# Optimization experiments

Measured on AMD Instinct MI355X. Metric: run time of the kernel, lower is better.

Reference implementation:

```python
import jax, jax.numpy as jnp
import numpy as np

D = 64        # d_model
HEADS = 4
DH = D // HEADS   # 16 per-head dim (shared QK)
DEPTH = 4
NHASH = 4
BS = 64       # bucket_size
FF = 4 * D
SELF_ATTN_VAL = -5e4  # reformer-pytorch TOKEN_SELF_ATTN_VALUE


def layer_norm(x, g, b, eps=1e-5):
    m = x.mean(-1, keepdims=True)
    v = ((x - m) ** 2).mean(-1, keepdims=True)
    return (x - m) * jax.lax.rsqrt(v + eps) * g + b


def lsh_attention(x, wqk, wv, wo_w, wo_b, rot):
    # x: (B, L, D); rot: (DH, NHASH, n_buckets//2) fixed random rotations
    B, L, _ = x.shape
    nb = L // BS                       # n_buckets
    qk = x @ wqk                        # shared query/key projection, no bias
    v = x @ wv

    def split_heads(t):
        return t.reshape(B, L, HEADS, DH).transpose(0, 2, 1, 3).reshape(B * HEADS, L, DH)

    qk, v = split_heads(qk), split_heads(v)
    Bh = B * HEADS

    # --- LSH hashing: argmax over [rot, -rot] projections ---
    rotated = jnp.einsum('btf,fhi->bhti', qk, rot)          # (Bh, NHASH, L, nb//2)
    rotated = jnp.concatenate([rotated, -rotated], axis=-1)  # (Bh, NHASH, L, nb)
    buckets = jnp.argmax(rotated, axis=-1)                   # (Bh, NHASH, L)
    offsets = (jnp.arange(NHASH) * nb)[None, :, None]
    buckets = (buckets + offsets).reshape(Bh, NHASH * L)

    # --- sort tokens by (bucket, position) ---
    ticker = jnp.arange(NHASH * L)
    bkt_t = buckets * L + (ticker % L)[None, :]
    sticker = jnp.argsort(bkt_t, axis=-1)
    undo_sort = jnp.argsort(sticker, axis=-1)
    st = sticker % L                                          # (Bh, NHASH*L)

    sqk = jnp.take_along_axis(qk, st[..., None], axis=1)
    sv = jnp.take_along_axis(v, st[..., None], axis=1)

    n_chunks = NHASH * nb
    bq_t = st.reshape(Bh, n_chunks, BS)
    bqk = sqk.reshape(Bh, n_chunks, BS, DH)
    bv = sv.reshape(Bh, n_chunks, BS, DH)
    bq = bqk
    bk = bqk / jnp.maximum(jnp.linalg.norm(bqk, axis=-1, keepdims=True), 1e-12)

    def look_one_back(t):
        return jnp.concatenate([t, jnp.roll(t, 1, axis=1)], axis=2)

    bk = look_one_back(bk)                    # (Bh, n_chunks, 2*BS, DH)
    bv = look_one_back(bv)
    bkv_t = look_one_back(bq_t[..., None])[..., 0]  # (Bh, n_chunks, 2*BS)

    dots = jnp.einsum('bcie,bcje->bcij', bq, bk) * (DH ** -0.5)
    self_mask = bq_t[:, :, :, None] == bkv_t[:, :, None, :]
    dots = jnp.where(self_mask, SELF_ATTN_VAL, dots)

    lse = jax.scipy.special.logsumexp(dots, axis=-1, keepdims=True)
    probs = jnp.exp(dots - lse)
    bo = jnp.einsum('bcij,bcje->bcie', probs, bv)

    so = bo.reshape(Bh, NHASH * L, DH)
    slog = lse.reshape(Bh, NHASH * L)
    o = jnp.take_along_axis(so, undo_sort[..., None], axis=1).reshape(Bh, NHASH, L, DH)
    logits = jnp.take_along_axis(slog, undo_sort, axis=1).reshape(Bh, NHASH, L, 1)

    # combine hash rounds weighted by their softmax normalizers
    w = jnp.exp(logits - jax.scipy.special.logsumexp(logits, axis=1, keepdims=True))
    out = (o * w).sum(axis=1)                 # (Bh, L, DH)
    out = out.reshape(B, HEADS, L, DH).transpose(0, 2, 1, 3).reshape(B, L, D)
    return out @ wo_w + wo_b


def feed_forward(x, w1, b1, w2, b2):
    return jax.nn.gelu(x @ w1 + b1, approximate=False) @ w2 + b2


def setup_inputs() -> dict:
    key = jax.random.key(0)
    ks = jax.random.split(key, 12)
    B = 16
    s = 0.02
    nb = 1280 // BS  # 20 buckets at padded seq len
    return {
        'wave': jax.random.normal(ks[0], (B, 2, 1250), jnp.float32),
        'in_w': jax.random.normal(ks[1], (2, D), jnp.float32) * s,
        'in_b': jnp.zeros((D,), jnp.float32),
        'ln1_g': jnp.ones((DEPTH, D), jnp.float32),
        'ln1_b': jnp.zeros((DEPTH, D), jnp.float32),
        'wqk': jax.random.normal(ks[2], (DEPTH, D, D), jnp.float32) * s,
        'wv': jax.random.normal(ks[3], (DEPTH, D, D), jnp.float32) * s,
        'wo_w': jax.random.normal(ks[4], (DEPTH, D, D), jnp.float32) * s,
        'wo_b': jnp.zeros((DEPTH, D), jnp.float32),
        'rot': jax.random.normal(ks[5], (DEPTH, DH, NHASH, nb // 2), jnp.float32),
        'ln2_g': jnp.ones((DEPTH, D), jnp.float32),
        'ln2_b': jnp.zeros((DEPTH, D), jnp.float32),
        'w1': jax.random.normal(ks[6], (DEPTH, D, FF), jnp.float32) * s,
        'b1': jnp.zeros((DEPTH, FF), jnp.float32),
        'w2': jax.random.normal(ks[7], (DEPTH, FF, D), jnp.float32) * s,
        'b2': jnp.zeros((DEPTH, D), jnp.float32),
        'out_w': jax.random.normal(ks[8], (D, 1), jnp.float32) * s,
        'out_b': jnp.zeros((1,), jnp.float32),
    }


def reference(wave, in_w, in_b, ln1_g, ln1_b, wqk, wv, wo_w, wo_b, rot,
              ln2_g, ln2_b, w1, b1, w2, b2, out_w, out_b):
    x = wave.transpose(0, 2, 1)               # (B, 1250, 2)
    L0 = x.shape[1]
    pad = (-L0) % (BS * 2)                    # pad to multiple of 128 -> 1280
    x = jnp.pad(x, ((0, 0), (0, pad), (0, 0)))
    x = x @ in_w + in_b                       # (B, L, D)

    # reversible sequence: y1 = x1 + attn(LN(x2)); y2 = x2 + ff(LN(y1))
    x1 = x2 = x
    for i in range(DEPTH):
        x1 = x1 + lsh_attention(layer_norm(x2, ln1_g[i], ln1_b[i]),
                                wqk[i], wv[i], wo_w[i], wo_b[i], rot[i])
        x2 = x2 + feed_forward(layer_norm(x1, ln2_g[i], ln2_b[i]),
                               w1[i], b1[i], w2[i], b2[i])
    x = (x1 + x2) * 0.5
    y = (x @ out_w + out_b)[..., 0]
    return y[:, :L0]
```

## Files before the change

### kernel.cpp

```cpp
#include <hip/hip_runtime.h>
#include <math.h>

#define LSEQ 1280
#define L0SEQ 1250
#define DM 64
#define NHEADS 4
#define DHD 16
#define NHASH 4
#define NBUK 20
#define NCHUNK 80
#define FFD 256
#define NBATCH 16
#define NBH 64

#define XSZ (NBATCH*LSEQ*DM)
#define QKSZ (NBH*LSEQ*DHD)
#define OHSZ (NBH*NHASH*LSEQ*DHD)
#define SLSZ (NBH*NHASH*LSEQ)

typedef __attribute__((ext_vector_type(8))) short frag_ab;
typedef __attribute__((ext_vector_type(4))) float frag_c;

union FU4 { uint4 v; frag_ab f; };

__device__ __forceinline__ unsigned rnbf(float x){
    unsigned b = __float_as_uint(x);
    return (b + 0x7fffu + ((b >> 16) & 1u)) >> 16;
}
__device__ __forceinline__ float bf2f(unsigned h){ return __uint_as_float(h << 16); }
__device__ __forceinline__ unsigned rot16(unsigned x){ return (x >> 16) | (x << 16); }
__device__ __forceinline__ uint4 rot16v(uint4 a){
    uint4 r; r.x=rot16(a.x); r.y=rot16(a.y); r.z=rot16(a.z); r.w=rot16(a.w); return r;
}

__device__ __forceinline__ void split3(float x, unsigned& h, unsigned& m, unsigned& l){
    unsigned bx = __float_as_uint(x);
    h = bx >> 16;
    float r = x - __uint_as_float(bx & 0xffff0000u);
    unsigned br = __float_as_uint(r);
    m = br >> 16;
    float r2 = r - __uint_as_float(br & 0xffff0000u);
    l = __float_as_uint(r2) >> 16;
}

__global__ __launch_bounds__(256) void k_init(
    const float* __restrict__ wave, const float* __restrict__ in_w, const float* __restrict__ in_b,
    float* __restrict__ x1, float* __restrict__ x2,
    const float* __restrict__ wo_w, const float* __restrict__ w1,
    const float* __restrict__ w2, unsigned* __restrict__ wsplit)
{
    if (blockIdx.x < 5120) {
        int idx = blockIdx.x * 256 + threadIdx.x;
        int d = idx & 63;
        int t = idx >> 6;
        int b = t / LSEQ;
        int tt = t % LSEQ;
        float v0 = 0.f, v1 = 0.f;
        if (tt < L0SEQ) {
            v0 = wave[(size_t)(b*2+0)*L0SEQ + tt];
            v1 = wave[(size_t)(b*2+1)*L0SEQ + tt];
        }
        float x = v0 * in_w[d] + v1 * in_w[64 + d] + in_b[d];
        x1[idx] = x;
        x2[idx] = x;
    } else {
        int gid = (blockIdx.x - 5120) * 256 + threadIdx.x;
        int l = gid / 36864;
        int r = gid % 36864;
        float src; unsigned* dst; int idx; int stride;
        if (r < 4096) {
            int k = r >> 6, n = r & 63;
            src = wo_w[l*4096 + k*64 + n];
            dst = wsplit + l*8192;
            idx = (((k>>4)*4 + (n>>4))*16 + (n&15))*16 + (k&15);
            stride = 4096;
        } else if (r < 20480) {
            int rr = r - 4096;
            int k = rr >> 8, n = rr & 255;
            src = w1[l*16384 + k*256 + n];
            dst = wsplit + 32768 + l*32768;
            idx = (((k>>4)*16 + (n>>4))*16 + (n&15))*16 + (k&15);
            stride = 16384;
        } else {
            int rr = r - 20480;
            int k = rr >> 6, n = rr & 63;
            src = w2[l*16384 + k*64 + n];
            dst = wsplit + 163840 + l*32768;
            idx = (((k>>4)*4 + (n>>4))*16 + (n&15))*16 + (k&15);
            stride = 16384;
        }
        unsigned h, m, lo;
        split3(src, h, m, lo);
        dst[idx]          = h | (m<<16);
        dst[idx + stride] = lo | (h<<16);
    }
}

__global__ __launch_bounds__(256) void k_qkv(
    const float* __restrict__ x2, const float* __restrict__ g, const float* __restrict__ bta,
    const float* __restrict__ wqk, const float* __restrict__ wv, const float* __restrict__ rot,
    unsigned* __restrict__ qkvs, int* __restrict__ buckets)
{
    __shared__ float xln[16][68];
    __shared__ float qkt[16][68];
    __shared__ float vvt[16][68];
    __shared__ float rots[640];
    int tid = threadIdx.x;
    int b  = blockIdx.x / 80;
    int t0 = (blockIdx.x % 80) * 16;
    int tok = tid >> 4;
    int cg  = tid & 15;
    int c4  = cg * 4;

    for (int i = tid; i < 640; i += 256) rots[i] = rot[i];

    float4 xv4 = *(const float4*)&x2[((size_t)b*LSEQ + t0 + tok)*DM + c4];
    float s = xv4.x + xv4.y + xv4.z + xv4.w;
    float ss = xv4.x*xv4.x + xv4.y*xv4.y + xv4.z*xv4.z + xv4.w*xv4.w;
    s  += __shfl_xor(s,1);  s  += __shfl_xor(s,2);  s  += __shfl_xor(s,4);  s  += __shfl_xor(s,8);
    ss += __shfl_xor(ss,1); ss += __shfl_xor(ss,2); ss += __shfl_xor(ss,4); ss += __shfl_xor(ss,8);
    float m = s * (1.f/64.f);
    float vr = ss * (1.f/64.f) - m*m;
    float rstd = 1.f / sqrtf(vr + 1e-5f);
    {
        float4 g4 = *(const float4*)&g[c4];
        float4 b4 = *(const float4*)&bta[c4];
        float4 o;
        o.x = (xv4.x-m)*rstd*g4.x + b4.x;
        o.y = (xv4.y-m)*rstd*g4.y + b4.y;
        o.z = (xv4.z-m)*rstd*g4.z + b4.z;
        o.w = (xv4.w-m)*rstd*g4.w + b4.w;
        *(float4*)&xln[tok][c4] = o;
    }
    __syncthreads();

    float aq[4] = {0,0,0,0}, av[4] = {0,0,0,0};
    for (int f = 0; f < 64; f++) {
        float4 wq4 = *(const float4*)&wqk[f*64 + c4];
        float4 wv4 = *(const float4*)&wv [f*64 + c4];
        float xv = xln[tok][f];
        aq[0] += xv*wq4.x; aq[1] += xv*wq4.y; aq[2] += xv*wq4.z; aq[3] += xv*wq4.w;
        av[0] += xv*wv4.x; av[1] += xv*wv4.y; av[2] += xv*wv4.z; av[3] += xv*wv4.w;
    }
    *(float4*)&qkt[tok][c4] = *(float4*)aq;
    *(float4*)&vvt[tok][c4] = *(float4*)av;
    __syncthreads();

    int p = tid >> 2;
    int ptok = p >> 2, head = p & 3;
    int sub = tid & 3;
    int e0 = sub * 4;
    int t = t0 + ptok;
    float4 qf4 = *(const float4*)&qkt[ptok][head*16 + e0];
    float nsq = qf4.x*qf4.x + qf4.y*qf4.y + qf4.z*qf4.z + qf4.w*qf4.w;
    nsq += __shfl_xor(nsq,1); nsq += __shfl_xor(nsq,2);
    float inv = 1.f / fmaxf(sqrtf(nsq), 1e-12f);
    float qe[4] = {qf4.x, qf4.y, qf4.z, qf4.w};
    unsigned wq[4], wk[4];
    #pragma unroll
    for (int i=0;i<4;i++){
        float xq = qe[i]*0.25f;
        unsigned qh = rnbf(xq);
        unsigned ql = rnbf(xq - bf2f(qh));
        wq[i] = qh | (ql<<16);
        float xk = qe[i]*inv;
        unsigned kh = rnbf(xk);
        unsigned kl = rnbf(xk - bf2f(kh));
        wk[i] = kh | (kl<<16);
    }
    float4 vf4 = *(const float4*)&vvt[ptok][head*16 + e0];
    float ve[4] = {vf4.x, vf4.y, vf4.z, vf4.w};
    unsigned wv1[4], wv3[4];
    #pragma unroll
    for (int i=0;i<4;i++){
        unsigned vh_, vm_, vl_;
        split3(ve[i], vh_, vm_, vl_);
        wv1[i] = vh_ | (vm_<<16);
        wv3[i] = vl_ | (vh_<<16);
    }
    size_t sb = (((size_t)(b*NHEADS+head))*LSEQ + t)*64;
    *(uint4*)&qkvs[sb + e0]      = *(uint4*)wq;
    *(uint4*)&qkvs[sb + 16 + e0] = *(uint4*)wk;
    *(uint4*)&qkvs[sb + 32 + e0] = *(uint4*)wv1;
    *(uint4*)&qkvs[sb + 48 + e0] = *(uint4*)wv3;

    float qf[16];
    {
        float4 a0 = *(const float4*)&qkt[ptok][head*16 + 0];
        float4 a1 = *(const float4*)&qkt[ptok][head*16 + 4];
        float4 a2 = *(const float4*)&qkt[ptok][head*16 + 8];
        float4 a3 = *(const float4*)&qkt[ptok][head*16 + 12];
        qf[0]=a0.x; qf[1]=a0.y; qf[2]=a0.z; qf[3]=a0.w;
        qf[4]=a1.x; qf[5]=a1.y; qf[6]=a1.z; qf[7]=a1.w;
        qf[8]=a2.x; qf[9]=a2.y; qf[10]=a2.z; qf[11]=a2.w;
        qf[12]=a3.x; qf[13]=a3.y; qf[14]=a3.z; qf[15]=a3.w;
    }
    int nh = sub;
    float rv[10];
    #pragma unroll
    for (int i=0;i<10;i++) {
        float acc = 0.f;
        #pragma unroll
        for (int f=0; f<16; f++) acc += qf[f]*rots[(f*NHASH+nh)*10 + i];
        rv[i] = acc;
    }
    float best = rv[0]; int bi = 0;
    #pragma unroll
    for (int i=1;i<10;i++) if (rv[i] > best) { best = rv[i]; bi = i; }
    #pragma unroll
    for (int i=0;i<10;i++) if (-rv[i] > best) { best = -rv[i]; bi = 10+i; }
    buckets[((size_t)(b*NHEADS+head)*NHASH + nh)*LSEQ + t] = bi;
}

__global__ __launch_bounds__(64) void k_sort(
    const int* __restrict__ buckets, int* __restrict__ sorted)
{
    __shared__ int hist[20];
    __shared__ int startl[20];
    int lane = threadIdx.x;
    int gidx = blockIdx.x;
    const int* bk = buckets + (size_t)gidx * LSEQ;
    int* dst = sorted + (size_t)gidx * LSEQ;
    if (lane < 20) hist[lane] = 0;
    __syncthreads();
    int myb[20];
    for (int ch = 0; ch < 20; ch++) {
        myb[ch] = bk[ch*64 + lane];
        atomicAdd(&hist[myb[ch]], 1);
    }
    __syncthreads();
    if (lane == 0) {
        int acc = 0;
        for (int b2 = 0; b2 < 20; b2++) { startl[b2] = acc; acc += hist[b2]; }
    }
    __syncthreads();
    unsigned long long below = (lane == 63) ? 0x7fffffffffffffffull
                                            : ((1ull << lane) - 1ull);
    for (int ch = 0; ch < 20; ch++) {
        int bv = myb[ch];
        unsigned long long mymask = 0, ownmask = 0;
        #pragma unroll
        for (int b2 = 0; b2 < 20; b2++) {
            unsigned long long m2 = __ballot(bv == b2);
            if (b2 == bv)   mymask  = m2;
            if (b2 == lane) ownmask = m2;
        }
        int rank = __popcll(mymask & below);
        int base = startl[bv];
        dst[base + rank] = ch*64 + lane;
        __syncthreads();
        if (lane < 20) startl[lane] += __popcll(ownmask);
        __syncthreads();
    }
}

__global__ __launch_bounds__(256) void k_attn(
    const unsigned* __restrict__ qkvs,
    const int* __restrict__ sorted, float* __restrict__ o_hash, float* __restrict__ slog)
{
    __shared__ __align__(16) unsigned SM[7904];
    unsigned* Va1 = SM;
    unsigned* Ka1 = SM + 2624;
    unsigned* Pa1 = SM + 2624;
    unsigned short* Vlh  = (unsigned short*)(SM + 5184);
    unsigned short* Pa2h = (unsigned short*)(SM + 6496);
    int* kposS = (int*)(SM + 7776);

    int tid = threadIdx.x;
    int bh = blockIdx.x & 63;
    int c  = blockIdx.x >> 6;
    int h  = c / NBUK, cc = c % NBUK;
    int cp = (c + NCHUNK - 1) % NCHUNK;
    int hp = cp / NBUK, ccp = cp % NBUK;

    int key = tid & 127;
    int pos = (key < 64)
        ? sorted[((size_t)bh*NHASH + h)*LSEQ + cc*64 + key]
        : sorted[((size_t)bh*NHASH + hp)*LSEQ + ccp*64 + (key-64)];
    size_t srow = ((size_t)bh*LSEQ + pos)*64;
    if (tid < 128) {
        kposS[key] = pos;
        const uint4* kr = (const uint4*)(qkvs + srow + 16);
        #pragma unroll
        for (int e4=0; e4<4; e4++)
            *(uint4*)&Ka1[key*20 + e4*4] = kr[e4];
    } else {
        const uint4* v1r = (const uint4*)(qkvs + srow + 32);
        const uint4* v3r = (const uint4*)(qkvs + srow + 48);
        int kt = key >> 4, jl = key & 15;
        int lb = kt*328 + jl;
        #pragma unroll
        for (int e4=0; e4<4; e4++){
            uint4 a = v1r[e4], c2 = v3r[e4];
            unsigned aa[4] = {a.x,a.y,a.z,a.w};
            unsigned cb[4] = {c2.x,c2.y,c2.z,c2.w};
            #pragma unroll
            for (int i=0;i<4;i++){
                int d = e4*4 + i;
                Va1[lb + d*20] = aa[i];
                Vlh[lb + d*20] = (unsigned short)(cb[i] & 0xffffu);
            }
        }
    }
    __syncthreads();

    int w = tid >> 6, lane = tid & 63;
    int quad = lane >> 4, col = lane & 15;

    int qgpos = kposS[16*w + col];
    FU4 QA;
    QA.v = *(const uint4*)(qkvs + ((size_t)bh*LSEQ + qgpos)*64 + quad*4);
    frag_ab qA = QA.f;

    frag_c acc[8];
    #pragma unroll
    for (int nt=0; nt<8; nt++){
        FU4 B1, B2;
        B1.v = *(const uint4*)&Ka1[(nt*16+col)*20 + 4*quad];
        B2.v = rot16v(B1.v);
        frag_c a = {0.f,0.f,0.f,0.f};
        a = __builtin_amdgcn_mfma_f32_16x16x32_bf16(qA, B1.f, a, 0, 0, 0);
        a = __builtin_amdgcn_mfma_f32_16x16x32_bf16(qA, B2.f, a, 0, 0, 0);
        acc[nt] = a;
    }
    int qp[4];
    #pragma unroll
    for (int reg=0; reg<4; reg++) qp[reg] = kposS[16*w + quad*4 + reg];
    #pragma unroll
    for (int nt=0; nt<8; nt++){
        int kp2 = kposS[nt*16 + col];
        #pragma unroll
        for (int reg=0; reg<4; reg++)
            if (kp2 == qp[reg]) acc[nt][reg] = -5e4f;
    }
    float mx[4] = {-3.4e38f,-3.4e38f,-3.4e38f,-3.4e38f};
    #pragma unroll
    for (int nt=0; nt<8; nt++)
        #pragma unroll
        for (int reg=0; reg<4; reg++) mx[reg] = fmaxf(mx[reg], acc[nt][reg]);
    #pragma unroll
    for (int reg=0; reg<4; reg++){
        float m2 = mx[reg];
        m2 = fmaxf(m2, __shfl_xor(m2, 1)); m2 = fmaxf(m2, __shfl_xor(m2, 2));
        m2 = fmaxf(m2, __shfl_xor(m2, 4)); m2 = fmaxf(m2, __shfl_xor(m2, 8));
        mx[reg] = m2;
    }
    float sm2[4] = {0.f,0.f,0.f,0.f};
    #pragma unroll
    for (int nt=0; nt<8; nt++)
        #pragma unroll
        for (int reg=0; reg<4; reg++){
            float e = __expf(acc[nt][reg] - mx[reg]);
            acc[nt][reg] = e; sm2[reg] += e;
        }
    #pragma unroll
    for (int reg=0; reg<4; reg++){
        float s2 = sm2[reg];
        s2 += __shfl_xor(s2, 1); s2 += __shfl_xor(s2, 2);
        s2 += __shfl_xor(s2, 4); s2 += __shfl_xor(s2, 8);
        sm2[reg] = s2;
    }
    float invs[4];
    #pragma unroll
    for (int reg=0; reg<4; reg++) invs[reg] = 1.f / sm2[reg];
    if (col == 0) {
        #pragma unroll
        for (int reg=0; reg<4; reg++)
            slog[((size_t)bh*NHASH + h)*LSEQ + qp[reg]] = mx[reg] + __logf(sm2[reg]);
    }

    frag_c o = {0.f,0.f,0.f,0.f};
    __syncthreads();
    #pragma unroll
    for (int pass=0; pass<4; pass++){
        #pragma unroll
        for (int t2=0; t2<2; t2++){
            int nt = pass*2 + t2;
            #pragma unroll
            for (int reg=0; reg<4; reg++){
                float p = acc[nt][reg] * invs[reg];
                unsigned ph_, pm_, pl_;
                split3(p, ph_, pm_, pl_);
                int idx = t2*1280 + (16*w + 4*quad + reg)*20 + col;
                Pa1[idx] = ph_ | (pm_<<16);
                Pa2h[idx] = (unsigned short)pl_;
            }
        }
        __syncthreads();
        #pragma unroll
        for (int t2=0; t2<2; t2++){
            int ktg = pass*2 + t2;
            FU4 A1, A2, B1, B2, B3;
            int pidx = t2*1280 + (16*w + col)*20 + 4*quad;
            A1.v = *(const uint4*)&Pa1[pidx];
            uint2 z = *(const uint2*)&Pa2h[pidx];
            A2.v.x = (A1.v.x & 0xffffu) | (z.x << 16);
            A2.v.y = (A1.v.y & 0xffffu) | (z.x & 0xffff0000u);
            A2.v.z = (A1.v.z & 0xffffu) | (z.y << 16);
            A2.v.w = (A1.v.w & 0xffffu) | (z.y & 0xffff0000u);
            int vidx = ktg*328 + col*20 + 4*quad;
            B1.v = *(const uint4*)&Va1[vidx];
            B2.v = rot16v(B1.v);
            uint2 zл = *(const uint2*)&Vlh[vidx];
            B3.v.x = (zл.x & 0xffffu) | (B1.v.x << 16);
            B3.v.y = (zл.x >> 16)     | (B1.v.y << 16);
            B3.v.z = (zл.y & 0xffffu) | (B1.v.z << 16);
            B3.v.w = (zл.y >> 16)     | (B1.v.w << 16);
            o = __builtin_amdgcn_mfma_f32_16x16x32_bf16(A1.f, B1.f, o, 0, 0, 0);
            o = __builtin_amdgcn_mfma_f32_16x16x32_bf16(A1.f, B2.f, o, 0, 0, 0);
            o = __builtin_amdgcn_mfma_f32_16x16x32_bf16(A2.f, B3.f, o, 0, 0, 0);
        }
        if (pass < 3) __syncthreads();
    }
    size_t obase = ((size_t)bh*NHASH + h)*LSEQ;
    #pragma unroll
    for (int reg=0; reg<4; reg++)
        o_hash[(obase + qp[reg])*DHD + col] = o[reg];
}

__global__ __launch_bounds__(256) void k_tail(
    const float* __restrict__ o_hash, const float* __restrict__ slog,
    const unsigned* __restrict__ wo_s, const float* __restrict__ wo_b,
    const float* __restrict__ g2, const float* __restrict__ b2t,
    const unsigned* __restrict__ w1_s, const float* __restrict__ b1,
    const unsigned* __restrict__ w2_s, const float* __restrict__ b2f,
    float* __restrict__ x1, float* __restrict__ x2,
    const float* __restrict__ out_w, const float* __restrict__ out_b,
    float* __restrict__ y, int do_out)
{
    __shared__ unsigned cA1[1024], cA2[1024];
    __shared__ unsigned xA1[1024], xA2[1024];
    __shared__ unsigned gA1[4096], gA2[4096];
    __shared__ float lnS[64], lnQ[64];
    float* red = (float*)gA1;

    int tid = threadIdx.x;
    int b  = blockIdx.x / 80;
    int t0 = (blockIdx.x % 80) * 16;
    int w = tid >> 6, lane = tid & 63;
    int quad = lane >> 4, col = lane & 15;

    {
        int tok = tid >> 4;
        int dg  = tid & 15;
        int d0  = dg * 4;
        int kt  = dg >> 2;
        int t = t0 + tok;
        int bh = b*NHEADS + kt;
        float sl[4];
        #pragma unroll
        for (int nh=0; nh<4; nh++) sl[nh] = slog[((size_t)bh*NHASH + nh)*LSEQ + t];
        float mx = fmaxf(fmaxf(sl[0],sl[1]), fmaxf(sl[2],sl[3]));
        float wgt[4]; float wsum = 0.f;
        #pragma unroll
        for (int nh=0; nh<4; nh++){ wgt[nh] = __expf(sl[nh]-mx); wsum += wgt[nh]; }
        float iv = 1.f/wsum;
        float a4[4] = {0.f,0.f,0.f,0.f};
        #pragma unroll
        for (int nh=0; nh<4; nh++){
            float4 oh = *(const float4*)&o_hash[(((size_t)bh*NHASH + nh)*LSEQ + t)*DHD + (d0 & 15)];
            float wn = wgt[nh]*iv;
            a4[0] += wn*oh.x; a4[1] += wn*oh.y; a4[2] += wn*oh.z; a4[3] += wn*oh.w;
        }
        int sw = (tok & 7) << 2;
        unsigned cw1[4], cw2[4];
        #pragma unroll
        for (int i=0;i<4;i++){
            unsigned h_, m_, l_;
            split3(a4[i], h_, m_, l_);
            cw1[i] = h_ | (m_<<16);
            cw2[i] = h_ | (l_<<16);
        }
        *(uint4*)&cA1[tok*64 + (d0 ^ sw)] = *(uint4*)cw1;
        *(uint4*)&cA2[tok*64 + (d0 ^ sw)] = *(uint4*)cw2;
    }
    __syncthreads();
    FU4 aA1[4], aA2[4];
    {
        int sw = (col & 7) << 2;
        #pragma unroll
        for (int kt=0; kt<4; kt++){
            int word = (kt*16 + quad*4) ^ sw;
            aA1[kt].v = *(const uint4*)&cA1[col*64 + word];
            aA2[kt].v = *(const uint4*)&cA2[col*64 + word];
        }
    }

    frag_c awo = {0.f,0.f,0.f,0.f};
    #pragma unroll
    for (int kt=0; kt<4; kt++){
        FU4 B1, B2, B3;
        int bidx = ((kt*4 + w)*16 + col)*16 + quad*4;
        B1.v = *(const uint4*)&wo_s[bidx];
        B2.v = rot16v(B1.v);
        B3.v = *(const uint4*)&wo_s[bidx + 4096];
        awo = __builtin_amdgcn_mfma_f32_16x16x32_bf16(aA1[kt].f, B1.f, awo, 0, 0, 0);
        awo = __builtin_amdgcn_mfma_f32_16x16x32_bf16(aA1[kt].f, B2.f, awo, 0, 0, 0);
        awo = __builtin_amdgcn_mfma_f32_16x16x32_bf16(aA2[kt].f, B3.f, awo, 0, 0, 0);
    }
    int cg = w*16 + col;
    float x1n[4];
    float s1[4], s2[4];
    {
        float wb = wo_b[cg];
        #pragma unroll
        for (int reg=0; reg<4; reg++){
            int rg = t0 + quad*4 + reg;
            size_t xi = ((size_t)b*LSEQ + rg)*DM + cg;
            float xv = x1[xi] + awo[reg] + wb;
            x1[xi] = xv;
            x1n[reg] = xv;
            s1[reg] = xv; s2[reg] = xv*xv;
        }
    }
    #pragma unroll
    for (int reg=0; reg<4; reg++){
        float a = s1[reg], q = s2[reg];
        a += __shfl_xor(a,1); a += __shfl_xor(a,2); a += __shfl_xor(a,4); a += __shfl_xor(a,8);
        q += __shfl_xor(q,1); q += __shfl_xor(q,2); q += __shfl_xor(q,4); q += __shfl_xor(q,8);
        s1[reg] = a; s2[reg] = q;
    }
    if (col == 0) {
        #pragma unroll
        for (int reg=0; reg<4; reg++){
            lnS[w*16 + quad*4 + reg] = s1[reg];
            lnQ[w*16 + quad*4 + reg] = s2[reg];
        }
    }
    __syncthreads();
    float mean[4], rstd[4];
    #pragma unroll
    for (int reg=0; reg<4; reg++){
        int tok = quad*4 + reg;
        float a = lnS[tok] + lnS[16+tok] + lnS[32+tok] + lnS[48+tok];
        float q = lnQ[tok] + lnQ[16+tok] + lnQ[32+tok] + lnQ[48+tok];
        mean[reg] = a*(1.f/64.f);
        float var = q*(1.f/64.f) - mean[reg]*mean[reg];
        rstd[reg] = 1.f/sqrtf(var + 1e-5f);
    }
    {
        float gv = g2[cg], bv = b2t[cg];
        #pragma unroll
        for (int reg=0; reg<4; reg++){
            int row = quad*4 + reg;
            float xv = (x1n[reg]-mean[reg])*rstd[reg]*gv + bv;
            unsigned h_, m_, l_;
            split3(xv, h_, m_, l_);
            int word = cg ^ ((row & 7) << 2);
            xA1[row*64 + word] = h_ | (m_<<16);
            xA2[row*64 + word] = h_ | (l_<<16);
        }
    }
    __syncthreads();
    FU4 xa1[4], xa2[4];
    {
        int sw = (col & 7) << 2;
        #pragma unroll
        for (int kt=0; kt<4; kt++){
            int word = (kt*16 + quad*4) ^ sw;
            xa1[kt].v = *(const uint4*)&xA1[col*64 + word];
            xa2[kt].v = *(const uint4*)&xA2[col*64 + word];
        }
    }

    unsigned* myg1 = gA1 + w*1024;
    unsigned* myg2 = gA2 + w*1024;
    #pragma unroll
    for (int ntl=0; ntl<4; ntl++){
        int nt = w*4 + ntl;
        frag_c a = {0.f,0.f,0.f,0.f};
        #pragma unroll
        for (int kt=0; kt<4; kt++){
            FU4 B1, B2, B3;
            int bidx = ((kt*16 + nt)*16 + col)*16 + quad*4;
            B1.v = *(const uint4*)&w1_s[bidx];
            B2.v = rot16v(B1.v);
            B3.v = *(const uint4*)&w1_s[bidx + 16384];
            a = __builtin_amdgcn_mfma_f32_16x16x32_bf16(xa1[kt].f, B1.f, a, 0, 0, 0);
            a = __builtin_amdgcn_mfma_f32_16x16x32_bf16(xa1[kt].f, B2.f, a, 0, 0, 0);
            a = __builtin_amdgcn_mfma_f32_16x16x32_bf16(xa2[kt].f, B3.f, a, 0, 0, 0);
        }
        float bb = b1[nt*16 + col];
        #pragma unroll
        for (int reg=0; reg<4; reg++){
            float xx = a[reg] + bb;
            float ge = 0.5f*xx*(1.f + erff(xx*0.70710678118654752f));
            unsigned h_, m_, l_;
            split3(ge, h_, m_, l_);
            int row = quad*4 + reg;
            int word = (ntl*16 + col) ^ ((row & 7) << 2);
            myg1[row*64 + word] = h_ | (m_<<16);
            myg2[row*64 + word] = h_ | (l_<<16);
        }
    }
    frag_c aw2[4] = {{0,0,0,0},{0,0,0,0},{0,0,0,0},{0,0,0,0}};
    {
        int sw = (col & 7) << 2;
        #pragma unroll
        for (int kt2=0; kt2<4; kt2++){
            FU4 A1, A2;
            int word = (kt2*16 + quad*4) ^ sw;
            A1.v = *(const uint4*)&myg1[col*64 + word];
            A2.v = *(const uint4*)&myg2[col*64 + word];
            int kg = w*4 + kt2;
            #pragma unroll
            for (int nt2=0; nt2<4; nt2++){
                FU4 B1, B2, B3;
                int bidx = ((kg*4 + nt2)*16 + col)*16 + quad*4;
                B1.v = *(const uint4*)&w2_s[bidx];
                B2.v = rot16v(B1.v);
                B3.v = *(const uint4*)&w2_s[bidx + 16384];
                aw2[nt2] = __builtin_amdgcn_mfma_f32_16x16x32_bf16(A1.f, B1.f, aw2[nt2], 0, 0, 0);
                aw2[nt2] = __builtin_amdgcn_mfma_f32_16x16x32_bf16(A1.f, B2.f, aw2[nt2], 0, 0, 0);
                aw2[nt2] = __builtin_amdgcn_mfma_f32_16x16x32_bf16(A2.f, B3.f, aw2[nt2], 0, 0, 0);
            }
        }
    }
    __syncthreads();
    #pragma unroll
    for (int nt2=0; nt2<4; nt2++)
        #pragma unroll
        for (int reg=0; reg<4; reg++)
            red[((w*4 + nt2)*4 + reg)*64 + lane] = aw2[nt2][reg];
    __syncthreads();
    float x2f[4];
    {
        float bb = b2f[cg];
        #pragma unroll
        for (int reg=0; reg<4; reg++){
            float v = red[((0*4 + w)*4 + reg)*64 + lane]
                    + red[((1*4 + w)*4 + reg)*64 + lane]
                    + red[((2*4 + w)*4 + reg)*64 + lane]
                    + red[((3*4 + w)*4 + reg)*64 + lane];
            int rg = t0 + quad*4 + reg;
            size_t xi = ((size_t)b*LSEQ + rg)*DM + cg;
            float nv = x2[xi] + v + bb;
            x2[xi] = nv;
            x2f[reg] = nv;
        }
    }
    if (do_out) {
        float ow = out_w[cg];
        float part[4];
        #pragma unroll
        for (int reg=0; reg<4; reg++){
            float p = (x1n[reg] + x2f[reg]) * 0.5f * ow;
            p += __shfl_xor(p,1); p += __shfl_xor(p,2); p += __shfl_xor(p,4); p += __shfl_xor(p,8);
            part[reg] = p;
        }
        __syncthreads();
        if (col == 0) {
            #pragma unroll
            for (int reg=0; reg<4; reg++)
                lnS[w*16 + quad*4 + reg] = part[reg];
        }
        __syncthreads();
        if (tid < 16) {
            int t = t0 + tid;
            if (t < L0SEQ) {
                float v2 = lnS[tid] + lnS[16+tid] + lnS[32+tid] + lnS[48+tid];
                y[(size_t)b*L0SEQ + t] = v2 + out_b[0];
            }
        }
    }
}

extern "C" void kernel_launch(void* const* d_in, const int* in_sizes, int n_in,
                              void* d_out, int out_size, void* d_ws, size_t ws_size,
                              hipStream_t stream)
{
    const float* wave  = (const float*)d_in[0];
    const float* in_w  = (const float*)d_in[1];
    const float* in_b  = (const float*)d_in[2];
    const float* ln1_g = (const float*)d_in[3];
    const float* ln1_b = (const float*)d_in[4];
    const float* wqk   = (const float*)d_in[5];
    const float* wv    = (const float*)d_in[6];
    const float* wo_w  = (const float*)d_in[7];
    const float* wo_b  = (const float*)d_in[8];
    const float* rot   = (const float*)d_in[9];
    const float* ln2_g = (const float*)d_in[10];
    const float* ln2_b = (const float*)d_in[11];
    const float* w1    = (const float*)d_in[12];
    const float* b1    = (const float*)d_in[13];
    const float* w2    = (const float*)d_in[14];
    const float* b2    = (const float*)d_in[15];
    const float* out_w = (const float*)d_in[16];
    const float* out_b = (const float*)d_in[17];
    float* y = (float*)d_out;

    float* ws = (float*)d_ws;
    float* x1      = ws;
    float* x2      = x1 + XSZ;
    unsigned* qkvs = (unsigned*)(x2 + XSZ);
    float* o_hash  = (float*)(qkvs + 4*QKSZ);
    float* slogb   = o_hash + OHSZ;
    int* buckets   = (int*)(slogb + SLSZ);
    int* sorted    = buckets + SLSZ;
    unsigned* wsplit = (unsigned*)(sorted + SLSZ);

    k_init<<<5696, 256, 0, stream>>>(wave, in_w, in_b, x1, x2, wo_w, w1, w2, wsplit);
    for (int layer = 0; layer < 4; layer++) {
        k_qkv<<<NBATCH*80, 256, 0, stream>>>(x2, ln1_g + layer*64, ln1_b + layer*64,
                                       wqk + layer*4096, wv + layer*4096, rot + layer*640,
                                       qkvs, buckets);
        k_sort<<<256, 64, 0, stream>>>(buckets, sorted);
        k_attn<<<NBH*NCHUNK, 256, 0, stream>>>(qkvs, sorted, o_hash, slogb);
        k_tail<<<NBATCH*LSEQ/16, 256, 0, stream>>>(o_hash, slogb,
                                        wsplit + layer*8192, wo_b + layer*64,
                                        ln2_g + layer*64, ln2_b + layer*64,
                                        wsplit + 32768 + layer*32768, b1 + layer*256,
                                        wsplit + 163840 + layer*32768, b2 + layer*64,
                                        x1, x2,
                                        out_w, out_b, y, (layer == 3) ? 1 : 0);
    }
}
```

Before: 562.3 us.

## Parallelize bucket sort across four waves with ballot-mask prefix counts

```diff
diff --git a/kernel.cpp b/kernel.cpp
--- a/kernel.cpp
+++ b/kernel.cpp
@@ -212,45 +212,53 @@
     buckets[((size_t)(b*NHEADS+head)*NHASH + nh)*LSEQ + t] = bi;
 }
 
-__global__ __launch_bounds__(64) void k_sort(
+__global__ __launch_bounds__(256) void k_sort(
     const int* __restrict__ buckets, int* __restrict__ sorted)
 {
-    __shared__ int hist[20];
+    __shared__ unsigned long long masks[20][20];
+    __shared__ int pre[20][20];
     __shared__ int startl[20];
-    int lane = threadIdx.x;
+    int tid = threadIdx.x;
+    int w = tid >> 6, lane = tid & 63;
     int gidx = blockIdx.x;
     const int* bk = buckets + (size_t)gidx * LSEQ;
     int* dst = sorted + (size_t)gidx * LSEQ;
-    if (lane < 20) hist[lane] = 0;
-    __syncthreads();
-    int myb[20];
-    for (int ch = 0; ch < 20; ch++) {
-        myb[ch] = bk[ch*64 + lane];
-        atomicAdd(&hist[myb[ch]], 1);
-    }
-    __syncthreads();
-    if (lane == 0) {
+
+    int myb[5];
+    #pragma unroll
+    for (int i = 0; i < 5; i++) {
+        int ch = w*5 + i;
+        int bv = bk[ch*64 + lane];
+        myb[i] = bv;
+        #pragma unroll
+        for (int b2 = 0; b2 < 20; b2++) {
+            unsigned long long m2 = __ballot(bv == b2);
+            if (lane == b2) masks[ch][b2] = m2;
+        }
+    }
+    __syncthreads();
+    if (tid < 20) {
+        int run = 0;
+        for (int ch = 0; ch < 20; ch++) {
+            pre[ch][tid] = run;
+            run += __popcll(masks[ch][tid]);
+        }
+        startl[tid] = run;
+    }
+    __syncthreads();
+    if (tid == 0) {
         int acc = 0;
-        for (int b2 = 0; b2 < 20; b2++) { startl[b2] = acc; acc += hist[b2]; }
+        for (int b2 = 0; b2 < 20; b2++) { int t = startl[b2]; startl[b2] = acc; acc += t; }
     }
     __syncthreads();
     unsigned long long below = (lane == 63) ? 0x7fffffffffffffffull
                                             : ((1ull << lane) - 1ull);
-    for (int ch = 0; ch < 20; ch++) {
-        int bv = myb[ch];
-        unsigned long long mymask = 0, ownmask = 0;
-        #pragma unroll
-        for (int b2 = 0; b2 < 20; b2++) {
-            unsigned long long m2 = __ballot(bv == b2);
-            if (b2 == bv)   mymask  = m2;
-            if (b2 == lane) ownmask = m2;
-        }
-        int rank = __popcll(mymask & below);
-        int base = startl[bv];
-        dst[base + rank] = ch*64 + lane;
-        __syncthreads();
-        if (lane < 20) startl[lane] += __popcll(ownmask);
-        __syncthreads();
+    #pragma unroll
+    for (int i = 0; i < 5; i++) {
+        int ch = w*5 + i;
+        int bv = myb[i];
+        int rank = startl[bv] + pre[ch][bv] + __popcll(masks[ch][bv] & below);
+        dst[rank] = ch*64 + lane;
     }
 }
 
@@ -401,11 +409,11 @@
             int vidx = ktg*328 + col*20 + 4*quad;
             B1.v = *(const uint4*)&Va1[vidx];
             B2.v = rot16v(B1.v);
-            uint2 zл = *(const uint2*)&Vlh[vidx];
-            B3.v.x = (zл.x & 0xffffu) | (B1.v.x << 16);
-            B3.v.y = (zл.x >> 16)     | (B1.v.y << 16);
-            B3.v.z = (zл.y & 0xffffu) | (B1.v.z << 16);
-            B3.v.w = (zл.y >> 16)     | (B1.v.w << 16);
+            uint2 zl = *(const uint2*)&Vlh[vidx];
+            B3.v.x = (zl.x & 0xffffu) | (B1.v.x << 16);
+            B3.v.y = (zl.x >> 16)     | (B1.v.y << 16);
+            B3.v.z = (zl.y & 0xffffu) | (B1.v.z << 16);
+            B3.v.w = (zl.y >> 16)     | (B1.v.w << 16);
             o = __builtin_amdgcn_mfma_f32_16x16x32_bf16(A1.f, B1.f, o, 0, 0, 0);
             o = __builtin_amdgcn_mfma_f32_16x16x32_bf16(A1.f, B2.f, o, 0, 0, 0);
             o = __builtin_amdgcn_mfma_f32_16x16x32_bf16(A2.f, B3.f, o, 0, 0, 0);
@@ -704,7 +712,7 @@
         k_qkv<<<NBATCH*80, 256, 0, stream>>>(x2, ln1_g + layer*64, ln1_b + layer*64,
                                        wqk + layer*4096, wv + layer*4096, rot + layer*640,
                                        qkvs, buckets);
-        k_sort<<<256, 64, 0, stream>>>(buckets, sorted);
+        k_sort<<<256, 256, 0, stream>>>(buckets, sorted);
         k_attn<<<NBH*NCHUNK, 256, 0, stream>>>(qkvs, sorted, o_hash, slogb);
         k_tail<<<NBATCH*LSEQ/16, 256, 0, stream>>>(o_hash, slogb,
                                         wsplit + layer*8192, wo_b + layer*64,
```

Measured after the change: 525.1 us. -6.6%, faster.
